# Optimization experiments

Measured on AMD Instinct MI355X. Metric: run time of the kernel, lower is better.

The kernel has to match this reference:

```python
import jax, jax.numpy as jnp
import numpy as np


def setup_inputs() -> dict:
    key = jax.random.key(0)
    k1, k2, k3, k4, k5 = jax.random.split(key, 5)
    N, V, C = 4096, 4, 256
    desc = jax.random.normal(k1, (N, V, C), dtype=jnp.float32)
    sf = jax.random.normal(k2, (N, V, C), dtype=jnp.float32)
    T = jax.random.normal(k3, (V, 4, 4), dtype=jnp.float32)
    W_rec = jax.random.normal(k4, (C, C), dtype=jnp.float32) * (1.0 / np.sqrt(C))
    W_T = jax.random.normal(k5, (32, C), dtype=jnp.float32) * (1.0 / np.sqrt(32))
    return {"desc": desc, "sf": sf, "T": T, "W_rec": W_rec, "W_T": W_T}


def reference(desc, sf, T, W_rec, W_T):
    # desc, sf: [N, V, C]; T: [V, 4, 4]
    N, V, C = desc.shape
    # F.normalize(desc, dim=2)
    dn = desc / jnp.maximum(jnp.linalg.norm(desc, axis=2, keepdims=True), 1e-12)
    ar = jnp.arange(N)
    loss_total = jnp.zeros((), dtype=desc.dtype)
    count = jnp.zeros((), dtype=desc.dtype)
    for i in range(V):
        for j in range(V):
            if i == j:
                continue
            di = dn[:, i, :]  # [N, C]
            dj = dn[:, j, :]  # [N, C]
            sim = di @ dj.T   # [N, N]
            idx_ij = jnp.argmax(sim, axis=1)
            idx_ji = jnp.argmax(sim, axis=0)
            mutual = (idx_ji[idx_ij] == ar)  # [N] bool, mutual nearest neighbors
            # kpnet.reconstruction(desc_i, T_i, T_j): linear, transform-conditioned
            rel = jnp.concatenate([T[i].ravel(), T[j].ravel()])  # [32]
            sf_recon = di @ W_rec + rel @ W_T  # [N, C]
            # torch.no_grad() block -> stop_gradient
            prob = jax.nn.softmax(sim, axis=1)
            sf_j_soft = jax.lax.stop_gradient(prob @ sf[:, j, :])  # [N, C]
            m = mutual.astype(desc.dtype)[:, None]  # [N, 1]
            n_sel = jnp.sum(m)
            sq = jnp.sum(((sf_recon - sf_j_soft) ** 2) * m)
            pair_loss = sq / jnp.maximum(n_sel * C, 1.0)  # masked MSE (mean over selected elems)
            valid = (n_sel > 0).astype(desc.dtype)
            loss_total = loss_total + valid * pair_loss
            count = count + valid
    return jnp.where(count > 0, loss_total / jnp.maximum(count, 1.0), 0.0 * jnp.sum(desc))
```

## Files before the change

### kernel.cpp

```cpp
#include <hip/hip_runtime.h>
#include <math.h>

#define N_ 4096
#define V_ 4
#define C_ 256

typedef __attribute__((ext_vector_type(8))) short bf16x8;
typedef __attribute__((ext_vector_type(4))) float f32x4;
typedef unsigned long long u64;

#define OFF_R      0ull
#define OFF_DNHI   16777216ull
#define OFF_DNLO   25165824ull
#define OFF_SFT    33554432ull
#define OFF_E      37748736ull
#define OFF_ET     88080384ull
#define OFF_WTH    138412032ull
#define OFF_WTL    138543104ull
#define OFF_ROWPK  138674176ull
#define OFF_COLPK  138870784ull
#define OFF_ROWSM  139067392ull
#define OFF_COLSM  139165696ull
#define OFF_RELWT  139264000ull
#define OFF_SQ     139280384ull
#define OFF_CNT    139280448ull

__device__ __forceinline__ unsigned short f2bf(float x) {
    unsigned int u = __float_as_uint(x);
    u += 0x7fffu + ((u >> 16) & 1u);
    return (unsigned short)(u >> 16);
}
__device__ __forceinline__ float bf2f(unsigned short h) {
    return __uint_as_float(((unsigned int)h) << 16);
}
__device__ __forceinline__ f32x4 mfma16(bf16x8 a, bf16x8 b, f32x4 c) {
    return __builtin_amdgcn_mfma_f32_16x16x32_bf16(a, b, c, 0, 0, 0);
}
__device__ __forceinline__ unsigned int pk4fp8(float x0, float x1, float x2, float x3) {
    int w = 0;
    w = __builtin_amdgcn_cvt_pk_fp8_f32(x0, x1, w, false);
    w = __builtin_amdgcn_cvt_pk_fp8_f32(x2, x3, w, true);
    return (unsigned int)w;
}
__device__ __forceinline__ double packkeyd(float v, int idx) {
    u64 k = ((u64)__float_as_uint(v) << 32) | (u64)(0xFFFFFFFFu - (unsigned)idx);
    return __longlong_as_double((long long)k);
}
__device__ __forceinline__ void dma16(const void* g, void* l) {
    __builtin_amdgcn_global_load_lds(
        (const __attribute__((address_space(1))) unsigned int*)g,
        (__attribute__((address_space(3))) unsigned int*)l, 16, 0, 0);
}

__global__ void normalize_k(const float* __restrict__ desc,
                            unsigned short* __restrict__ dnh, unsigned short* __restrict__ dnl) {
    int row = blockIdx.x;
    int n = row >> 2, v = row & 3;
    int c = threadIdx.x;
    float x = desc[(size_t)row * C_ + c];
    __shared__ float red[256];
    red[c] = x * x;
    __syncthreads();
    for (int s = 128; s > 0; s >>= 1) {
        if (c < s) red[c] += red[c + s];
        __syncthreads();
    }
    float inv = 1.0f / fmaxf(sqrtf(red[0]), 1e-12f);
    float y = x * inv;
    size_t o = ((size_t)v * N_ + n) * C_ + c;
    unsigned short h = f2bf(y);
    dnh[o] = h;
    dnl[o] = f2bf(y - bf2f(h));
}

__global__ void wrecT_k(const float* __restrict__ W, unsigned short* __restrict__ WTh,
                        unsigned short* __restrict__ WTl) {
    __shared__ float Tt[64 * 65];
    int k0 = blockIdx.x * 64, c0 = blockIdx.y * 64;
    int t = threadIdx.x;
    int kr = t >> 2, cq = (t & 3) * 16;
    const float* src = W + (size_t)(k0 + kr) * C_ + c0 + cq;
    for (int u = 0; u < 16; ++u) Tt[(cq + u) * 65 + kr] = src[u];
    __syncthreads();
    int cr = t >> 2, kq = (t & 3) * 16;
    unsigned short th[16] __attribute__((aligned(16)));
    unsigned short tl[16] __attribute__((aligned(16)));
    for (int u = 0; u < 16; ++u) {
        float x = Tt[cr * 65 + kq + u];
        unsigned short h = f2bf(x);
        th[u] = h; tl[u] = f2bf(x - bf2f(h));
    }
    size_t o = (size_t)(c0 + cr) * C_ + k0 + kq;
    *(uint4*)(WTh + o) = *(const uint4*)th;
    *(uint4*)(WTh + o + 8) = *(const uint4*)(th + 8);
    *(uint4*)(WTl + o) = *(const uint4*)tl;
    *(uint4*)(WTl + o + 8) = *(const uint4*)(tl + 8);
}

__global__ __launch_bounds__(256) void rmatmul_k(
    const unsigned short* __restrict__ Ah, const unsigned short* __restrict__ Al,
    const unsigned short* __restrict__ Bh, const unsigned short* __restrict__ Bl,
    float* __restrict__ R) {
    __shared__ unsigned short smem[4 * 128 * 40];
    unsigned short* sAh = smem;
    unsigned short* sAl = sAh + 128 * 40;
    unsigned short* sBh = sAl + 128 * 40;
    unsigned short* sBl = sBh + 128 * 40;
    int tid = threadIdx.x;
    int c0 = blockIdx.x * 128, m0 = blockIdx.y * 128;
    int w = tid >> 6, l = tid & 63, wm = w & 1, wn = w >> 1;
    int mr = l & 15, q = l >> 4;
    f32x4 acc[4][4];
#pragma unroll
    for (int a = 0; a < 4; ++a)
#pragma unroll
        for (int b = 0; b < 4; ++b)
#pragma unroll
            for (int u = 0; u < 4; ++u) acc[a][b][u] = 0.f;
    int r = tid >> 1, h = (tid & 1) * 16;
    for (int k0 = 0; k0 < C_; k0 += 32) {
        size_t ga = (size_t)(m0 + r) * C_ + k0 + h;
        size_t gb = (size_t)(c0 + r) * C_ + k0 + h;
        uint4 a0 = *(const uint4*)(Ah + ga);
        uint4 a1 = *(const uint4*)(Ah + ga + 8);
        uint4 a2 = *(const uint4*)(Al + ga);
        uint4 a3 = *(const uint4*)(Al + ga + 8);
        uint4 b0 = *(const uint4*)(Bh + gb);
        uint4 b1 = *(const uint4*)(Bh + gb + 8);
        uint4 b2 = *(const uint4*)(Bl + gb);
        uint4 b3 = *(const uint4*)(Bl + gb + 8);
        *(uint4*)(sAh + r * 40 + h)     = a0;
        *(uint4*)(sAh + r * 40 + h + 8) = a1;
        *(uint4*)(sAl + r * 40 + h)     = a2;
        *(uint4*)(sAl + r * 40 + h + 8) = a3;
        *(uint4*)(sBh + r * 40 + h)     = b0;
        *(uint4*)(sBh + r * 40 + h + 8) = b1;
        *(uint4*)(sBl + r * 40 + h)     = b2;
        *(uint4*)(sBl + r * 40 + h + 8) = b3;
        __syncthreads();
        bf16x8 fah[4], fal[4], fbh[4], fbl[4];
#pragma unroll
        for (int ti = 0; ti < 4; ++ti) {
            int row = wm * 64 + ti * 16 + mr;
            fah[ti] = *(const bf16x8*)(sAh + row * 40 + q * 8);
            fal[ti] = *(const bf16x8*)(sAl + row * 40 + q * 8);
        }
#pragma unroll
        for (int tj = 0; tj < 4; ++tj) {
            int row = wn * 64 + tj * 16 + mr;
            fbh[tj] = *(const bf16x8*)(sBh + row * 40 + q * 8);
            fbl[tj] = *(const bf16x8*)(sBl + row * 40 + q * 8);
        }
#pragma unroll
        for (int ti = 0; ti < 4; ++ti)
#pragma unroll
            for (int tj = 0; tj < 4; ++tj) acc[ti][tj] = mfma16(fah[ti], fbh[tj], acc[ti][tj]);
#pragma unroll
        for (int ti = 0; ti < 4; ++ti)
#pragma unroll
            for (int tj = 0; tj < 4; ++tj) acc[ti][tj] = mfma16(fah[ti], fbl[tj], acc[ti][tj]);
#pragma unroll
        for (int ti = 0; ti < 4; ++ti)
#pragma unroll
            for (int tj = 0; tj < 4; ++tj) acc[ti][tj] = mfma16(fal[ti], fbh[tj], acc[ti][tj]);
        __syncthreads();
    }
#pragma unroll
    for (int ti = 0; ti < 4; ++ti)
#pragma unroll
        for (int tj = 0; tj < 4; ++tj) {
            int c = c0 + wn * 64 + tj * 16 + mr;
#pragma unroll
            for (int rg = 0; rg < 4; ++rg) {
                int m = m0 + wm * 64 + ti * 16 + q * 4 + rg;
                R[(size_t)m * C_ + c] = acc[ti][tj][rg];
            }
        }
}

__global__ void relwt_k(const float* __restrict__ T, const float* __restrict__ WT,
                        float* __restrict__ relwt) {
    int p = blockIdx.x; int i = p >> 2, j = p & 3;
    if (i == j) return;
    int c = threadIdx.x;
    float acc = 0.f;
    for (int k = 0; k < 16; ++k) acc += T[i * 16 + k] * WT[(size_t)k * C_ + c];
    for (int k = 0; k < 16; ++k) acc += T[j * 16 + k] * WT[(size_t)(16 + k) * C_ + c];
    relwt[(size_t)p * C_ + c] = acc;
}

__global__ void sfT_k(const float* __restrict__ sf, unsigned char* __restrict__ sf8T) {
    __shared__ float Tt[64 * 65];
    int n0 = blockIdx.x * 64, c0 = blockIdx.y * 64, v = blockIdx.z;
    int t = threadIdx.x;
    int nr = t >> 2, cq = (t & 3) * 16;
    const float* src = sf + ((size_t)(n0 + nr) * V_ + v) * C_ + c0 + cq;
    for (int u = 0; u < 16; ++u) Tt[(cq + u) * 65 + nr] = src[u];
    __syncthreads();
    int cr = t >> 2, nq = (t & 3) * 16;
    unsigned int wb[4];
#pragma unroll
    for (int g = 0; g < 4; ++g) {
        const float* p = Tt + cr * 65 + nq + g * 4;
        wb[g] = pk4fp8(p[0], p[1], p[2], p[3]);
    }
    unsigned char* dst = sf8T + ((size_t)v * C_ + c0 + cr) * N_ + n0 + nq;
    *(uint4*)dst = make_uint4(wb[0], wb[1], wb[2], wb[3]);
}

__global__ void zero_k(u64* rowPk, u64* colPk, float* rowSm, float* colSm,
                       float* sq, int* cnt) {
    int idx = blockIdx.x * 256 + threadIdx.x;
    rowPk[idx] = 0ull; colPk[idx] = 0ull;
    rowSm[idx] = 0.f;  colSm[idx] = 0.f;
    if (idx < 16) { sq[idx] = 0.f; cnt[idx] = 0; }
}

__device__ __forceinline__ void dma_stage(const unsigned short* A_h, const unsigned short* A_l,
                                          const unsigned short* B_h, const unsigned short* B_l,
                                          char* lbase, int w, int laneOff, int k0) {
#pragma unroll
    for (int gg = 0; gg < 2; ++gg) {
        int g = w * 2 + gg;
        size_t go = (size_t)g * 16 * C_ + k0 + laneOff;
        char* lb = lbase + g * 1024;
        dma16(A_h + go, lb);
        dma16(A_l + go, lb + 8192);
        dma16(B_h + go, lb + 16384);
        dma16(B_l + go, lb + 24576);
    }
}

__global__ __launch_bounds__(256, 4) void sim_mfma_k(
    const unsigned short* __restrict__ dnh, const unsigned short* __restrict__ dnl,
    int ipack, int jpack, unsigned char* __restrict__ E8b, unsigned char* __restrict__ ET8b,
    u64* __restrict__ rowPkB, float* __restrict__ rowSmB,
    u64* __restrict__ colPkB, float* __restrict__ colSmB, int slotBase) {
    __shared__ char smem[33792];

    int zp = blockIdx.z;
    int iv = (ipack >> (8 * zp)) & 15;
    int jv = (jpack >> (8 * zp)) & 15;
    unsigned char* E8  = E8b  + (size_t)zp * N_ * N_;
    unsigned char* ET8 = ET8b + (size_t)zp * N_ * N_;
    int slot = slotBase + zp;
    u64*   rowPk = rowPkB + (size_t)slot * N_;
    float* rowSm = rowSmB + (size_t)slot * N_;
    u64*   colPk = colPkB + (size_t)slot * N_;
    float* colSm = colSmB + (size_t)slot * N_;

    int tid = threadIdx.x;
    int n0 = blockIdx.x * 128, m0 = blockIdx.y * 128;
    int w = tid >> 6, l = tid & 63;
    int wm = w & 1, wn = w >> 1;
    int mr = l & 15, q = l >> 4;
    int sl = q ^ ((mr >> 1) & 3);

    int rowoff = l >> 2;
    int laneOff = rowoff * C_ + (((l & 3) ^ ((rowoff >> 1) & 3)) * 8);

    const unsigned short* Ah0 = dnh + (size_t)iv * N_ * C_ + (size_t)m0 * C_;
    const unsigned short* Al0 = dnl + (size_t)iv * N_ * C_ + (size_t)m0 * C_;
    const unsigned short* Bh0 = dnh + (size_t)jv * N_ * C_ + (size_t)n0 * C_;
    const unsigned short* Bl0 = dnl + (size_t)jv * N_ * C_ + (size_t)n0 * C_;

    f32x4 acc[4][4];
#pragma unroll
    for (int a = 0; a < 4; ++a)
#pragma unroll
        for (int b = 0; b < 4; ++b)
#pragma unroll
            for (int u = 0; u < 4; ++u) acc[a][b][u] = 0.f;

    for (int kc = 0; kc < 8; ++kc) {
        dma_stage(Ah0, Al0, Bh0, Bl0, smem, w, laneOff, kc * 32);
        __syncthreads();
        const unsigned short* sb = (const unsigned short*)smem;
        bf16x8 ah[4], al[4], bh[4], bl[4];
#pragma unroll
        for (int ti = 0; ti < 4; ++ti) {
            int row = wm * 64 + ti * 16 + mr;
            ah[ti] = *(const bf16x8*)(sb + row * 32 + sl * 8);
            al[ti] = *(const bf16x8*)(sb + 4096 + row * 32 + sl * 8);
        }
#pragma unroll
        for (int tj = 0; tj < 4; ++tj) {
            int row = wn * 64 + tj * 16 + mr;
            bh[tj] = *(const bf16x8*)(sb + 8192 + row * 32 + sl * 8);
            bl[tj] = *(const bf16x8*)(sb + 12288 + row * 32 + sl * 8);
        }
#pragma unroll
        for (int ti = 0; ti < 4; ++ti)
#pragma unroll
            for (int tj = 0; tj < 4; ++tj) {
                acc[ti][tj] = mfma16(ah[ti], bh[tj], acc[ti][tj]);
                acc[ti][tj] = mfma16(ah[ti], bl[tj], acc[ti][tj]);
                acc[ti][tj] = mfma16(al[ti], bh[tj], acc[ti][tj]);
            }
        __syncthreads();
    }

#pragma unroll
    for (int ti = 0; ti < 4; ++ti)
#pragma unroll
        for (int tj = 0; tj < 4; ++tj)
#pragma unroll
            for (int rg = 0; rg < 4; ++rg)
                acc[ti][tj][rg] = __expf(acc[ti][tj][rg]);

    unsigned short* S16 = (unsigned short*)smem;
#pragma unroll
    for (int ti = 0; ti < 4; ++ti)
#pragma unroll
        for (int tj = 0; tj < 4; ++tj)
#pragma unroll
            for (int rg = 0; rg < 4; ++rg)
                S16[(wm * 64 + ti * 16 + q * 4 + rg) * 132 + wn * 64 + tj * 16 + mr] =
                    f2bf(acc[ti][tj][rg]);

#pragma unroll
    for (int ti = 0; ti < 4; ++ti)
#pragma unroll
        for (int rg = 0; rg < 4; ++rg) {
            double best = 0.0;
#pragma unroll
            for (int tj = 0; tj < 4; ++tj)
                best = fmax(best, packkeyd(acc[ti][tj][rg], n0 + wn * 64 + tj * 16 + mr));
            best = fmax(best, __shfl_xor(best, 1));
            best = fmax(best, __shfl_xor(best, 2));
            best = fmax(best, __shfl_xor(best, 4));
            best = fmax(best, __shfl_xor(best, 8));
            if (mr == 0)
                atomicMax(rowPk + m0 + wm * 64 + ti * 16 + q * 4 + rg,
                          (u64)__double_as_longlong(best));
        }
#pragma unroll
    for (int tj = 0; tj < 4; ++tj) {
        double best = 0.0;
#pragma unroll
        for (int ti = 0; ti < 4; ++ti)
#pragma unroll
            for (int rg = 0; rg < 4; ++rg)
                best = fmax(best, packkeyd(acc[ti][tj][rg], m0 + wm * 64 + ti * 16 + q * 4 + rg));
        best = fmax(best, __shfl_xor(best, 16));
        best = fmax(best, __shfl_xor(best, 32));
        if (q == 0)
            atomicMax(colPk + n0 + wn * 64 + tj * 16 + mr,
                      (u64)__double_as_longlong(best));
    }
    __syncthreads();

    {
        int rr = tid & 127, hf = tid >> 7;
        const unsigned short* Sr = S16 + rr * 132 + hf * 64;
        unsigned char* dst = E8 + (size_t)(m0 + rr) * N_ + n0 + hf * 64;
        float sum = 0.f;
#pragma unroll
        for (int g = 0; g < 4; ++g) {
            unsigned int wb[4];
#pragma unroll
            for (int h2 = 0; h2 < 4; ++h2) {
                ushort4 vv = *(const ushort4*)(Sr + g * 16 + h2 * 4);
                float f0 = bf2f(vv.x), f1 = bf2f(vv.y), f2 = bf2f(vv.z), f3 = bf2f(vv.w);
                sum += (f0 + f1) + (f2 + f3);
                wb[h2] = pk4fp8(f0, f1, f2, f3);
            }
            *(uint4*)(dst + g * 16) = make_uint4(wb[0], wb[1], wb[2], wb[3]);
        }
        atomicAdd(rowSm + m0 + rr, sum);
    }
    {
        int cc = tid & 127, hf = tid >> 7;
        unsigned char* dst = ET8 + (size_t)(n0 + cc) * N_ + m0 + hf * 64;
        float sum = 0.f;
#pragma unroll
        for (int g = 0; g < 4; ++g) {
            unsigned int wb[4];
#pragma unroll
            for (int h2 = 0; h2 < 4; ++h2) {
                int rb = hf * 64 + g * 16 + h2 * 4;
                float f0 = bf2f(S16[(rb + 0) * 132 + cc]);
                float f1 = bf2f(S16[(rb + 1) * 132 + cc]);
                float f2 = bf2f(S16[(rb + 2) * 132 + cc]);
                float f3 = bf2f(S16[(rb + 3) * 132 + cc]);
                sum += (f0 + f1) + (f2 + f3);
                wb[h2] = pk4fp8(f0, f1, f2, f3);
            }
            *(uint4*)(dst + g * 16) = make_uint4(wb[0], wb[1], wb[2], wb[3]);
        }
        atomicAdd(colSm + n0 + cc, sum);
    }
}

__global__ __launch_bounds__(256) void p2_k(
    const unsigned char* __restrict__ E8b, const unsigned char* __restrict__ ET8b,
    const unsigned char* __restrict__ sf8T, int ipack, int jpack,
    const u64* __restrict__ rowPkB, const float* __restrict__ rowSmB,
    const u64* __restrict__ colPkB, const float* __restrict__ colSmB, int slotBase,
    const float* __restrict__ R, const float* __restrict__ relwt,
    float* __restrict__ pairSq, int* __restrict__ pairCnt) {
    __shared__ unsigned char sA[64 * 80];
    __shared__ unsigned char sB[128 * 80];
    __shared__ float red[256];
    __shared__ int   mutS[64];
    __shared__ float invS[64];
    int tid = threadIdx.x;
    int ct = blockIdx.x & 1, mt = blockIdx.x >> 1;
    int d = blockIdx.y & 1, zp = blockIdx.y >> 1;
    int iv = (ipack >> (8 * zp)) & 15;
    int jv = (jpack >> (8 * zp)) & 15;
    int slot = slotBase + zp;
    const unsigned char* A = (d ? ET8b : E8b) + (size_t)zp * N_ * N_;
    const unsigned char* B = sf8T + (size_t)(d ? iv : jv) * C_ * N_;
    const u64* faPk = (d ? colPkB : rowPkB) + (size_t)slot * N_;
    const u64* baPk = (d ? rowPkB : colPkB) + (size_t)slot * N_;
    const float* sumE = (d ? colSmB : rowSmB) + (size_t)slot * N_;
    const float* Rr = R + (size_t)(d ? jv : iv) * N_ * C_;
    int pid = d ? (jv * 4 + iv) : (iv * 4 + jv);
    int c0 = ct * 128, m0 = mt * 64;
    int w = tid >> 6, l = tid & 63, wm = w & 1, wn = w >> 1;
    int mr = l & 15, q = l >> 4;
    if (tid < 64) {
        int y = m0 + tid;
        unsigned faIdx = 0xFFFFFFFFu - (unsigned)(faPk[y] & 0xFFFFFFFFull);
        unsigned baIdx = 0xFFFFFFFFu - (unsigned)(baPk[faIdx] & 0xFFFFFFFFull);
        mutS[tid] = (baIdx == (unsigned)y) ? 1 : 0;
        invS[tid] = 1.0f / sumE[y];
    }
    f32x4 acc[2][4];
#pragma unroll
    for (int a = 0; a < 2; ++a)
#pragma unroll
        for (int b = 0; b < 4; ++b)
#pragma unroll
            for (int u = 0; u < 4; ++u) acc[a][b][u] = 0.f;

    int ra = tid >> 2, ka = (tid & 3) * 16;
    int rb = tid >> 1, kbb = (tid & 1) * 32;
    const unsigned char* Arow = A + (size_t)(m0 + ra) * N_ + ka;
    const unsigned char* Brow = B + (size_t)(c0 + rb) * N_ + kbb;
    uint4 pa  = *(const uint4*)(Arow);
    uint4 pb0 = *(const uint4*)(Brow);
    uint4 pb1 = *(const uint4*)(Brow + 16);
    for (int k0 = 0; k0 < N_; k0 += 64) {
        *(uint4*)(sA + ra * 80 + ka)       = pa;
        *(uint4*)(sB + rb * 80 + kbb)      = pb0;
        *(uint4*)(sB + rb * 80 + kbb + 16) = pb1;
        __syncthreads();
        int kn = k0 + 64;
        if (kn < N_) {
            pa  = *(const uint4*)(Arow + kn);
            pb0 = *(const uint4*)(Brow + kn);
            pb1 = *(const uint4*)(Brow + kn + 16);
        }
#pragma unroll
        for (int ksub = 0; ksub < 64; ksub += 32) {
            long af[2], bf[4];
#pragma unroll
            for (int ti = 0; ti < 2; ++ti)
                af[ti] = *(const long*)(sA + (wm * 32 + ti * 16 + mr) * 80 + ksub + q * 8);
#pragma unroll
            for (int tj = 0; tj < 4; ++tj)
                bf[tj] = *(const long*)(sB + (wn * 64 + tj * 16 + mr) * 80 + ksub + q * 8);
#pragma unroll
            for (int ti = 0; ti < 2; ++ti)
#pragma unroll
                for (int tj = 0; tj < 4; ++tj)
                    acc[ti][tj] = __builtin_amdgcn_mfma_f32_16x16x32_fp8_fp8(
                        af[ti], bf[tj], acc[ti][tj], 0, 0, 0);
        }
        __syncthreads();
    }
    const float* rw = relwt + (size_t)pid * C_;
    float local = 0.f;
#pragma unroll
    for (int ti = 0; ti < 2; ++ti)
#pragma unroll
        for (int tj = 0; tj < 4; ++tj) {
            int c = c0 + wn * 64 + tj * 16 + mr;
            float rwc = rw[c];
#pragma unroll
            for (int rg = 0; rg < 4; ++rg) {
                int ml = wm * 32 + ti * 16 + q * 4 + rg;
                if (mutS[ml]) {
                    int m = m0 + ml;
                    float soft = acc[ti][tj][rg] * invS[ml];
                    float dv = Rr[(size_t)m * C_ + c] + rwc - soft;
                    local += dv * dv;
                }
            }
        }
    red[tid] = local;
    __syncthreads();
    for (int s = 128; s > 0; s >>= 1) {
        if (tid < s) red[tid] += red[tid + s];
        __syncthreads();
    }
    if (tid == 0) {
        atomicAdd(pairSq + pid, red[0]);
        if (ct == 0) {
            int cnt = 0;
            for (int u = 0; u < 64; ++u) cnt += mutS[u];
            atomicAdd(pairCnt + pid, cnt);
        }
    }
}

__global__ void final_k(const float* __restrict__ sq, const int* __restrict__ cnt,
                        float* __restrict__ out) {
    if (threadIdx.x == 0 && blockIdx.x == 0) {
        float loss = 0.f, count = 0.f;
        for (int p = 0; p < 16; ++p) {
            int i = p >> 2, j = p & 3;
            if (i == j) continue;
            float ns = (float)cnt[p];
            if (ns > 0.f) { loss += sq[p] / fmaxf(ns * (float)C_, 1.0f); count += 1.f; }
        }
        out[0] = (count > 0.f) ? loss / count : 0.f;
    }
}

extern "C" void kernel_launch(void* const* d_in, const int* in_sizes, int n_in,
                              void* d_out, int out_size, void* d_ws, size_t ws_size,
                              hipStream_t stream) {
    const float* desc = (const float*)d_in[0];
    const float* sf   = (const float*)d_in[1];
    const float* T    = (const float*)d_in[2];
    const float* Wrec = (const float*)d_in[3];
    const float* WT   = (const float*)d_in[4];
    float* out = (float*)d_out;
    char* ws = (char*)d_ws;

    float*          R     = (float*)(ws + OFF_R);
    unsigned short* dnh   = (unsigned short*)(ws + OFF_DNHI);
    unsigned short* dnl   = (unsigned short*)(ws + OFF_DNLO);
    unsigned char*  sf8T  = (unsigned char*)(ws + OFF_SFT);
    unsigned char*  E8b   = (unsigned char*)(ws + OFF_E);
    unsigned char*  ET8b  = (unsigned char*)(ws + OFF_ET);
    unsigned short* WTh   = (unsigned short*)(ws + OFF_WTH);
    unsigned short* WTl   = (unsigned short*)(ws + OFF_WTL);
    u64*   rowPk = (u64*)(ws + OFF_ROWPK);
    u64*   colPk = (u64*)(ws + OFF_COLPK);
    float* rowSm = (float*)(ws + OFF_ROWSM);
    float* colSm = (float*)(ws + OFF_COLSM);
    float* relwt = (float*)(ws + OFF_RELWT);
    float* pairSq = (float*)(ws + OFF_SQ);
    int*   pairCnt = (int*)(ws + OFF_CNT);

    normalize_k<<<N_ * V_, 256, 0, stream>>>(desc, dnh, dnl);
    wrecT_k<<<dim3(4, 4), 256, 0, stream>>>(Wrec, WTh, WTl);
    rmatmul_k<<<dim3(2, 128), 256, 0, stream>>>(dnh, dnl, WTh, WTl, R);
    sfT_k<<<dim3(64, 4, 4), 256, 0, stream>>>(sf, sf8T);
    relwt_k<<<16, 256, 0, stream>>>(T, WT, relwt);
    zero_k<<<96, 256, 0, stream>>>(rowPk, colPk, rowSm, colSm, pairSq, pairCnt);

    const int ip[2] = { 0 | (0 << 8) | (0 << 16), 1 | (1 << 8) | (2 << 16) };
    const int jp[2] = { 1 | (2 << 8) | (3 << 16), 2 | (3 << 8) | (3 << 16) };
    for (int b = 0; b < 2; ++b) {
        sim_mfma_k<<<dim3(32, 32, 3), 256, 0, stream>>>(
            dnh, dnl, ip[b], jp[b], E8b, ET8b, rowPk, rowSm, colPk, colSm, b * 3);
        p2_k<<<dim3(128, 6), 256, 0, stream>>>(
            E8b, ET8b, sf8T, ip[b], jp[b], rowPk, rowSm, colPk, colSm, b * 3,
            R, relwt, pairSq, pairCnt);
    }
    final_k<<<1, 64, 0, stream>>>(pairSq, pairCnt, out);
}
```

Baseline: 585.7 us.

## Coalesce E/ET fp8 stores with nontemporal writes, block swizzle, and MFMA priority

Rewrites the epilogue of the similarity kernel so eight threads cover each 128-byte row segment, giving coalesced 16-byte nontemporal stores for both E and its transpose. The transpose is now built by rewriting the tile into shared memory in transposed order rather than read with strided column accesses. Row sums are reduced with shuffles, which cuts the number of atomics. It also remaps block indices so consecutive blocks share B tiles, changes the shared-memory pitch to 134, and raises wave priority around the MFMA loop. The cost is an extra shared-memory pass and barriers.

```diff
diff --git a/kernel.cpp b/kernel.cpp
--- a/kernel.cpp
+++ b/kernel.cpp
@@ -7,6 +7,7 @@
 
 typedef __attribute__((ext_vector_type(8))) short bf16x8;
 typedef __attribute__((ext_vector_type(4))) float f32x4;
+typedef __attribute__((ext_vector_type(4))) unsigned int u32x4;
 typedef unsigned long long u64;
 
 #define OFF_R      0ull
@@ -50,6 +51,11 @@
     __builtin_amdgcn_global_load_lds(
         (const __attribute__((address_space(1))) unsigned int*)g,
         (__attribute__((address_space(3))) unsigned int*)l, 16, 0, 0);
+}
+__device__ __forceinline__ void st_nt16(void* p, unsigned int a, unsigned int b,
+                                        unsigned int c, unsigned int d) {
+    u32x4 v = { a, b, c, d };
+    __builtin_nontemporal_store(v, (u32x4*)p);
 }
 
 __global__ void normalize_k(const float* __restrict__ desc,
@@ -231,12 +237,14 @@
     }
 }
 
+#define SP_ 134
+
 __global__ __launch_bounds__(256, 4) void sim_mfma_k(
     const unsigned short* __restrict__ dnh, const unsigned short* __restrict__ dnl,
     int ipack, int jpack, unsigned char* __restrict__ E8b, unsigned char* __restrict__ ET8b,
     u64* __restrict__ rowPkB, float* __restrict__ rowSmB,
     u64* __restrict__ colPkB, float* __restrict__ colSmB, int slotBase) {
-    __shared__ char smem[33792];
+    __shared__ char smem[128 * SP_ * 2];
 
     int zp = blockIdx.z;
     int iv = (ipack >> (8 * zp)) & 15;
@@ -250,7 +258,10 @@
     float* colSm = colSmB + (size_t)slot * N_;
 
     int tid = threadIdx.x;
-    int n0 = blockIdx.x * 128, m0 = blockIdx.y * 128;
+    int idl = blockIdx.x + (blockIdx.y << 5);
+    int kq_ = idl >> 3;
+    int m0 = ((idl & 7) * 4 + (kq_ & 3)) * 128;
+    int n0 = (kq_ >> 2) * 128;
     int w = tid >> 6, l = tid & 63;
     int wm = w & 1, wn = w >> 1;
     int mr = l & 15, q = l >> 4;
@@ -289,6 +300,7 @@
             bh[tj] = *(const bf16x8*)(sb + 8192 + row * 32 + sl * 8);
             bl[tj] = *(const bf16x8*)(sb + 12288 + row * 32 + sl * 8);
         }
+        __builtin_amdgcn_s_setprio(1);
 #pragma unroll
         for (int ti = 0; ti < 4; ++ti)
 #pragma unroll
@@ -297,6 +309,7 @@
                 acc[ti][tj] = mfma16(ah[ti], bl[tj], acc[ti][tj]);
                 acc[ti][tj] = mfma16(al[ti], bh[tj], acc[ti][tj]);
             }
+        __builtin_amdgcn_s_setprio(0);
         __syncthreads();
     }
 
@@ -315,7 +328,7 @@
         for (int tj = 0; tj < 4; ++tj)
 #pragma unroll
             for (int rg = 0; rg < 4; ++rg)
-                S16[(wm * 64 + ti * 16 + q * 4 + rg) * 132 + wn * 64 + tj * 16 + mr] =
+                S16[(wm * 64 + ti * 16 + q * 4 + rg) * SP_ + wn * 64 + tj * 16 + mr] =
                     f2bf(acc[ti][tj][rg]);
 
 #pragma unroll
@@ -351,44 +364,58 @@
     __syncthreads();
 
     {
-        int rr = tid & 127, hf = tid >> 7;
-        const unsigned short* Sr = S16 + rr * 132 + hf * 64;
-        unsigned char* dst = E8 + (size_t)(m0 + rr) * N_ + n0 + hf * 64;
-        float sum = 0.f;
-#pragma unroll
-        for (int g = 0; g < 4; ++g) {
+        int rsub = tid >> 3, seg = tid & 7;
+#pragma unroll
+        for (int it = 0; it < 4; ++it) {
+            int row = it * 32 + rsub;
+            const unsigned short* Sr = S16 + row * SP_ + seg * 16;
+            float sum = 0.f;
             unsigned int wb[4];
 #pragma unroll
             for (int h2 = 0; h2 < 4; ++h2) {
-                ushort4 vv = *(const ushort4*)(Sr + g * 16 + h2 * 4);
+                ushort4 vv = *(const ushort4*)(Sr + h2 * 4);
                 float f0 = bf2f(vv.x), f1 = bf2f(vv.y), f2 = bf2f(vv.z), f3 = bf2f(vv.w);
                 sum += (f0 + f1) + (f2 + f3);
                 wb[h2] = pk4fp8(f0, f1, f2, f3);
             }
-            *(uint4*)(dst + g * 16) = make_uint4(wb[0], wb[1], wb[2], wb[3]);
-        }
-        atomicAdd(rowSm + m0 + rr, sum);
-    }
+            st_nt16(E8 + (size_t)(m0 + row) * N_ + n0 + seg * 16, wb[0], wb[1], wb[2], wb[3]);
+            sum += __shfl_xor(sum, 1);
+            sum += __shfl_xor(sum, 2);
+            sum += __shfl_xor(sum, 4);
+            if (seg == 0) atomicAdd(rowSm + m0 + row, sum);
+        }
+    }
+    __syncthreads();
+#pragma unroll
+    for (int ti = 0; ti < 4; ++ti)
+#pragma unroll
+        for (int tj = 0; tj < 4; ++tj)
+#pragma unroll
+            for (int rg = 0; rg < 4; ++rg)
+                S16[(wn * 64 + tj * 16 + mr) * SP_ + wm * 64 + ti * 16 + q * 4 + rg] =
+                    f2bf(acc[ti][tj][rg]);
+    __syncthreads();
     {
-        int cc = tid & 127, hf = tid >> 7;
-        unsigned char* dst = ET8 + (size_t)(n0 + cc) * N_ + m0 + hf * 64;
-        float sum = 0.f;
-#pragma unroll
-        for (int g = 0; g < 4; ++g) {
+        int rsub = tid >> 3, seg = tid & 7;
+#pragma unroll
+        for (int it = 0; it < 4; ++it) {
+            int nn = it * 32 + rsub;
+            const unsigned short* Sr = S16 + nn * SP_ + seg * 16;
+            float sum = 0.f;
             unsigned int wb[4];
 #pragma unroll
             for (int h2 = 0; h2 < 4; ++h2) {
-                int rb = hf * 64 + g * 16 + h2 * 4;
-                float f0 = bf2f(S16[(rb + 0) * 132 + cc]);
-                float f1 = bf2f(S16[(rb + 1) * 132 + cc]);
-                float f2 = bf2f(S16[(rb + 2) * 132 + cc]);
-                float f3 = bf2f(S16[(rb + 3) * 132 + cc]);
+                ushort4 vv = *(const ushort4*)(Sr + h2 * 4);
+                float f0 = bf2f(vv.x), f1 = bf2f(vv.y), f2 = bf2f(vv.z), f3 = bf2f(vv.w);
                 sum += (f0 + f1) + (f2 + f3);
                 wb[h2] = pk4fp8(f0, f1, f2, f3);
             }
-            *(uint4*)(dst + g * 16) = make_uint4(wb[0], wb[1], wb[2], wb[3]);
-        }
-        atomicAdd(colSm + n0 + cc, sum);
+            st_nt16(ET8 + (size_t)(n0 + nn) * N_ + m0 + seg * 16, wb[0], wb[1], wb[2], wb[3]);
+            sum += __shfl_xor(sum, 1);
+            sum += __shfl_xor(sum, 2);
+            sum += __shfl_xor(sum, 4);
+            if (seg == 0) atomicAdd(colSm + n0 + nn, sum);
+        }
     }
 }
 
```

After: 941.8 us. 1.61x slower.
